# Kernel optimization log

Hardware: AMD Instinct MI355X
Metric: run time of the kernel (lower is better)

Reference implementation:

```python
import jax, jax.numpy as jnp
import numpy as np

HEADS = 8
EPS = 1e-5


def _attn_axis(x, axis, wq, wkv, wout, bout):
    # x: (B, C, X, Y, Z); self-attention along `axis`, channels at dim 1.
    perm = [0] + [d for d in (2, 3, 4) if d != axis] + [axis, 1]
    xp = jnp.transpose(x, perm)                    # (B, o1, o2, T, C)
    B, o1, o2, T, C = xp.shape
    xf = xp.reshape(B * o1 * o2, T, C)
    q = xf @ wq.T                                  # (Bf, T, C), no bias
    k, v = jnp.split(xf @ wkv.T, 2, axis=-1)
    e = C // HEADS
    sh = lambda t: t.reshape(t.shape[0], T, HEADS, e)
    q, k, v = sh(q), sh(k), sh(v)
    dots = jnp.einsum('bihe,bjhe->bhij', q, k) * (e ** -0.5)
    attn = jax.nn.softmax(dots, axis=-1)
    o = jnp.einsum('bhij,bjhe->bihe', attn, v).reshape(B * o1 * o2, T, C)
    o = (o @ wout.T + bout).reshape(B, o1, o2, T, C)
    inv = tuple(int(i) for i in np.argsort(perm))
    return jnp.transpose(o, inv)


def _ln(x, g, b):
    m = jnp.mean(x, -1, keepdims=True)
    v = jnp.mean((x - m) ** 2, -1, keepdims=True)
    return (x - m) * jax.lax.rsqrt(v + EPS) * g + b


def setup_inputs() -> dict:
    key = jax.random.key(0)
    B, C, X, Y, Z = 2, 128, 48, 48, 48
    ks = iter(jax.random.split(key, 32))
    n = lambda shape, s=0.02: jax.random.normal(next(ks), shape, jnp.float32) * s
    inp = {}
    inp['x'] = jax.random.normal(next(ks), (B, C, X, Y, Z), jnp.float32)
    inp['px'] = jax.random.normal(next(ks), (1, C, X, 1, 1), jnp.float32)
    inp['py'] = jax.random.normal(next(ks), (1, C, 1, Y, 1), jnp.float32)
    inp['pz'] = jax.random.normal(next(ks), (1, C, 1, 1, Z), jnp.float32)
    for i in range(3):
        inp[f'wq{i}'] = n((C, C))
        inp[f'wkv{i}'] = n((2 * C, C))
        inp[f'wout{i}'] = n((C, C))
        inp[f'bout{i}'] = jnp.zeros((C,), jnp.float32)
    inp['ln_g'] = jnp.ones((C,), jnp.float32)
    inp['ln_b'] = jnp.zeros((C,), jnp.float32)
    inp['w1'] = n((C, C)); inp['b1'] = jnp.zeros((C,), jnp.float32)
    inp['w2'] = n((C, C)); inp['b2'] = jnp.zeros((C,), jnp.float32)
    return inp


def reference(x, px, py, pz,
              wq0, wkv0, wout0, bout0,
              wq1, wkv1, wout1, bout1,
              wq2, wkv2, wout2, bout2,
              ln_g, ln_b, w1, b1, w2, b2):
    # source: x += pos_embedding(x); pos_embedding(x) returns x + px + py + pz
    x = x + (x + px + py + pz)
    a = (_attn_axis(x, 2, wq0, wkv0, wout0, bout0)
         + _attn_axis(x, 3, wq1, wkv1, wout1, bout1)
         + _attn_axis(x, 4, wq2, wkv2, wout2, bout2))
    x = a + x                                      # residual (dropout = identity)
    x = jnp.transpose(x, (0, 2, 3, 4, 1))          # channels last
    x = _ln(x, ln_g, ln_b)
    res = x
    h = jax.nn.relu(x @ w1.T + b1)
    h = h @ w2.T + b2
    x = _ln(h + res, ln_g, ln_b)                   # same LayerNorm weights reused
    return jnp.transpose(x, (0, 4, 1, 2, 3))
```

## Files before the change

kernel.cpp:

```cpp
#include <hip/hip_runtime.h>
#include <hip/hip_bf16.h>

typedef __attribute__((ext_vector_type(8))) short short8;
typedef __attribute__((ext_vector_type(4))) short short4v;
typedef __attribute__((ext_vector_type(4))) float floatx4;

#define XSTR 136
#define VSTR 56
#define SSTR 132
#define MSTR 129

static __device__ __forceinline__ short f2b(float f) {
    __hip_bfloat16 h = __float2bfloat16(f);
    return *reinterpret_cast<short*>(&h);
}
static __device__ __forceinline__ float b2f(short s) {
    unsigned int u = ((unsigned int)(unsigned short)s) << 16;
    return __uint_as_float(u);
}

__global__ __launch_bounds__(256) void prep_weights(
    const float* __restrict__ wq0, const float* __restrict__ wkv0,
    const float* __restrict__ wq1, const float* __restrict__ wkv1,
    const float* __restrict__ wq2, const float* __restrict__ wkv2,
    const float* __restrict__ wout0, const float* __restrict__ wout1,
    const float* __restrict__ wout2, const float* __restrict__ w1,
    const float* __restrict__ w2, short* __restrict__ dst)
{
    const int g = blockIdx.x * 256 + threadIdx.x;
    const float* wqs[3]  = { wq0, wq1, wq2 };
    const float* wkvs[3] = { wkv0, wkv1, wkv2 };
    const float* rest[5] = { wout0, wout1, wout2, w1, w2 };
    float val;
    if (g < 147456) {
        const int a = g / 49152, l = g % 49152;
        val = (l < 16384) ? wqs[a][l] : wkvs[a][l - 16384];
    } else {
        const int l = g - 147456;
        val = rest[l >> 14][l & 16383];
    }
    dst[g] = f2b(val);
}

__global__ __launch_bounds__(256) void prep_x2(
    const float* __restrict__ x, const float* __restrict__ px,
    const float* __restrict__ py, const float* __restrict__ pz,
    short* __restrict__ x2b)
{
    __shared__ float tile[128 * 49];
    const int s = blockIdx.x, tid = threadIdx.x;
    const int b = s / 2304, rr = s % 2304, xx = rr / 48, yy = rr % 48;
    for (int f = tid; f < 1536; f += 256) {
        const int c = f / 12, z4 = (f % 12) * 4;
        const floatx4 xv = *(const floatx4*)(x + (long)(b * 128 + c) * 110592 + xx * 2304 + yy * 48 + z4);
        const float pxy = px[c * 48 + xx] + py[c * 48 + yy];
        #pragma unroll
        for (int j = 0; j < 4; ++j)
            tile[c * 49 + z4 + j] = 2.0f * xv[j] + pxy + pz[c * 48 + z4 + j];
    }
    __syncthreads();
    const long tb = (long)b * 110592 + xx * 2304 + yy * 48;
    for (int f = tid; f < 1536; f += 256) {
        const int t = f >> 5, c4 = (f & 31) << 2;
        short4v pk;
        #pragma unroll
        for (int j = 0; j < 4; ++j) pk[j] = f2b(tile[(c4 + j) * 49 + t]);
        *(short4v*)(x2b + (tb + t) * 128 + c4) = pk;
    }
}

template<int AXIS, int ACC>
__global__ __launch_bounds__(512, 4)
void attn_axis(const short* __restrict__ x2b, const short* __restrict__ wcat,
               const short* __restrict__ woutb, const float* __restrict__ bout,
               short* __restrict__ Ab)
{
    __shared__ __align__(16) char SM[67840];
    short* xs  = (short*)SM;
    short* qs  = (short*)(SM + 13056);
    short* ks  = (short*)(SM + 26112);
    short* vs  = (short*)(SM + 39168);
    short* pb  = (short*)(SM + 53504);
    float* stg = (float*)(SM + 13056);

    const int tid  = threadIdx.x;
    const int lane = tid & 63;
    const int wave = tid >> 6;
    const int l15  = lane & 15;
    const int quad = lane >> 4;

    const int s = blockIdx.x;
    const int b = s / 2304, rr = s % 2304, u = rr / 48, v = rr % 48;
    long base; int stride;
    if (AXIS == 0) { base = (long)b * 110592 + u * 48   + v; stride = 2304; }
    else           { base = (long)b * 110592 + u * 2304 + v; stride = 48;   }

    short4v apre[3];
    if (ACC) {
        #pragma unroll
        for (int i = 0; i < 3; ++i) {
            const int f = tid + i * 512;
            const int t = f >> 5, c4 = (f & 31) << 2;
            apre[i] = *(const short4v*)(Ab + (base + (long)t * stride) * 128 + c4);
        }
    }
    short8 bcur[4], bnext[4];
    {
        const short* wp = wcat + (wave * 48 + l15) * 128 + quad * 8;
        #pragma unroll
        for (int k = 0; k < 4; ++k) bcur[k] = *(const short8*)(wp + k * 32);
    }

    for (int f = tid; f < 1536; f += 512) {
        const int t = f >> 5, c4 = (f & 31) << 2;
        *(short4v*)(xs + t * XSTR + c4) =
            *(const short4v*)(x2b + (base + (long)t * stride) * 128 + c4);
    }
    __syncthreads();

    short8 af[3][4];
    #pragma unroll
    for (int mt = 0; mt < 3; ++mt)
        #pragma unroll
        for (int k = 0; k < 4; ++k)
            af[mt][k] = *(const short8*)(xs + (mt * 16 + l15) * XSTR + k * 32 + quad * 8);

    for (int nti = 0; nti < 3; ++nti) {
        const int nt = wave * 3 + nti;
        const int n  = nt * 16 + l15;
        if (nti < 2) {
            const short* wp = wcat + ((nt + 1) * 16 + l15) * 128 + quad * 8;
            #pragma unroll
            for (int k = 0; k < 4; ++k) bnext[k] = *(const short8*)(wp + k * 32);
        }
        floatx4 acc[3] = {{0,0,0,0},{0,0,0,0},{0,0,0,0}};
        #pragma unroll
        for (int mt = 0; mt < 3; ++mt)
            #pragma unroll
            for (int k = 0; k < 4; ++k)
                acc[mt] = __builtin_amdgcn_mfma_f32_16x16x32_bf16(af[mt][k], bcur[k], acc[mt], 0, 0, 0);
        #pragma unroll
        for (int mt = 0; mt < 3; ++mt) {
            const int rbase = mt * 16 + quad * 4;
            if (n < 128) {
                #pragma unroll
                for (int g = 0; g < 4; ++g)
                    qs[(rbase + g) * XSTR + n] = f2b(acc[mt][g] * 0.25f);
            } else if (n < 256) {
                #pragma unroll
                for (int g = 0; g < 4; ++g)
                    ks[(rbase + g) * XSTR + (n - 128)] = f2b(acc[mt][g]);
            } else {
                short4v pk;
                #pragma unroll
                for (int g = 0; g < 4; ++g) pk[g] = f2b(acc[mt][g]);
                *(short4v*)(vs + (n - 256) * VSTR + rbase) = pk;
            }
        }
        #pragma unroll
        for (int k = 0; k < 4; ++k) bcur[k] = bnext[k];
    }
    __syncthreads();

    short* pbw = pb + wave * (16 * VSTR);
    const short8 Z8 = {0,0,0,0,0,0,0,0};
    for (int task = wave; task < 24; task += 8) {
        const int h  = task / 3;
        const int mt = task - h * 3;
        const int hb = h * 16;
        short8 aq = Z8;
        if (quad < 2) aq = *(const short8*)(qs + (mt * 16 + l15) * XSTR + hb + quad * 8);
        floatx4 sc[3];
        #pragma unroll
        for (int nt = 0; nt < 3; ++nt) {
            short8 bk = Z8;
            if (quad < 2) bk = *(const short8*)(ks + (nt * 16 + l15) * XSTR + hb + quad * 8);
            floatx4 z = {0,0,0,0};
            sc[nt] = __builtin_amdgcn_mfma_f32_16x16x32_bf16(aq, bk, z, 0, 0, 0);
        }
        #pragma unroll
        for (int g = 0; g < 4; ++g) {
            float m = fmaxf(fmaxf(sc[0][g], sc[1][g]), sc[2][g]);
            m = fmaxf(m, __shfl_xor(m, 1, 64));
            m = fmaxf(m, __shfl_xor(m, 2, 64));
            m = fmaxf(m, __shfl_xor(m, 4, 64));
            m = fmaxf(m, __shfl_xor(m, 8, 64));
            const float e0 = __expf(sc[0][g] - m);
            const float e1 = __expf(sc[1][g] - m);
            const float e2 = __expf(sc[2][g] - m);
            float ssum = e0 + e1 + e2;
            ssum += __shfl_xor(ssum, 1, 64);
            ssum += __shfl_xor(ssum, 2, 64);
            ssum += __shfl_xor(ssum, 4, 64);
            ssum += __shfl_xor(ssum, 8, 64);
            const float inv = 1.0f / ssum;
            short* prow = pbw + (quad * 4 + g) * VSTR;
            prow[l15]      = f2b(e0 * inv);
            prow[16 + l15] = f2b(e1 * inv);
            prow[32 + l15] = f2b(e2 * inv);
        }
        floatx4 o = {0,0,0,0};
        {
            short8 ap = *(const short8*)(pbw + l15 * VSTR + quad * 8);
            short8 bv = *(const short8*)(vs + (hb + l15) * VSTR + quad * 8);
            o = __builtin_amdgcn_mfma_f32_16x16x32_bf16(ap, bv, o, 0, 0, 0);
            short8 ap1 = Z8, bv1 = Z8;
            if (quad < 2) {
                ap1 = *(const short8*)(pbw + l15 * VSTR + 32 + quad * 8);
                bv1 = *(const short8*)(vs + (hb + l15) * VSTR + 32 + quad * 8);
            }
            o = __builtin_amdgcn_mfma_f32_16x16x32_bf16(ap1, bv1, o, 0, 0, 0);
        }
        #pragma unroll
        for (int g = 0; g < 4; ++g)
            xs[(mt * 16 + quad * 4 + g) * XSTR + hb + l15] = f2b(o[g]);
    }
    __syncthreads();

    #pragma unroll
    for (int mt = 0; mt < 3; ++mt)
        #pragma unroll
        for (int k = 0; k < 4; ++k)
            af[mt][k] = *(const short8*)(xs + (mt * 16 + l15) * XSTR + k * 32 + quad * 8);

    {
        const int n = wave * 16 + l15;
        short8 bf_[4];
        #pragma unroll
        for (int k = 0; k < 4; ++k)
            bf_[k] = *(const short8*)(woutb + n * 128 + k * 32 + quad * 8);
        floatx4 acc[3] = {{0,0,0,0},{0,0,0,0},{0,0,0,0}};
        #pragma unroll
        for (int mt = 0; mt < 3; ++mt)
            #pragma unroll
            for (int k = 0; k < 4; ++k)
                acc[mt] = __builtin_amdgcn_mfma_f32_16x16x32_bf16(af[mt][k], bf_[k], acc[mt], 0, 0, 0);
        const float bo = bout[n];
        #pragma unroll
        for (int mt = 0; mt < 3; ++mt)
            #pragma unroll
            for (int g = 0; g < 4; ++g)
                stg[(mt * 16 + quad * 4 + g) * SSTR + n] = acc[mt][g] + bo;
    }
    __syncthreads();

    #pragma unroll
    for (int i = 0; i < 3; ++i) {
        const int f = tid + i * 512;
        const int t = f >> 5, c4 = (f & 31) << 2;
        const long gi = (base + (long)t * stride) * 128 + c4;
        const floatx4 vv = *(const floatx4*)(stg + t * SSTR + c4);
        short4v out4;
        if (ACC) {
            #pragma unroll
            for (int j = 0; j < 4; ++j) out4[j] = f2b(b2f(apre[i][j]) + vv[j]);
        } else {
            #pragma unroll
            for (int j = 0; j < 4; ++j) out4[j] = f2b(vv[j]);
        }
        *(short4v*)(Ab + gi) = out4;
    }
}

static __device__ __forceinline__ void ln_stats129(const float* xr, float* mean_,
                                                   float* rstd_, int tid)
{
    if (tid < 192) {
        const int r = tid >> 2, p = tid & 3;
        const float* row = xr + r * MSTR + p * 32;
        float s1 = 0.f, s2 = 0.f;
        #pragma unroll
        for (int c = 0; c < 32; ++c) { const float xv = row[c]; s1 += xv; s2 += xv * xv; }
        s1 += __shfl_xor(s1, 1, 64); s1 += __shfl_xor(s1, 2, 64);
        s2 += __shfl_xor(s2, 1, 64); s2 += __shfl_xor(s2, 2, 64);
        if (p == 0) {
            const float m = s1 * (1.f / 128.f);
            mean_[r] = m;
            rstd_[r] = rsqrtf(s2 * (1.f / 128.f) - m * m + 1e-5f);
        }
    }
}

__global__ __launch_bounds__(512, 4)
void attn2_mlp(const short* __restrict__ x2b, const short* __restrict__ Ab,
               const short* __restrict__ wcat, const short* __restrict__ woutb,
               const float* __restrict__ bout,
               const float* __restrict__ ln_g, const float* __restrict__ ln_b,
               const short* __restrict__ w1b, const float* __restrict__ b1,
               const short* __restrict__ w2b, const float* __restrict__ b2,
               float* __restrict__ out)
{
    __shared__ __align__(16) char SM[70272];
    short* xs   = (short*)SM;
    short* qs   = (short*)(SM + 13056);
    short* ks   = (short*)(SM + 26112);
    short* vs   = (short*)(SM + 39168);
    short* pb   = (short*)(SM + 53504);
    short* ob   = xs;
    float* xr   = (float*)(SM + 13056);
    short* lnb  = (short*)(SM + 39168);
    short* hbuf = xs;
    float* gs   = (float*)(SM + 67840);
    float* bs   = (float*)(SM + 68352);
    float* b1s  = (float*)(SM + 68864);
    float* b2s  = (float*)(SM + 69376);
    float* mean_ = (float*)(SM + 69888);
    float* rstd_ = (float*)(SM + 70080);

    const int tid  = threadIdx.x;
    const int lane = tid & 63;
    const int wave = tid >> 6;
    const int l15  = lane & 15;
    const int quad = lane >> 4;

    const int s = blockIdx.x;
    const int b = s / 2304, rr = s % 2304, xx = rr / 48, yy = rr % 48;
    const long tb = (long)b * 110592 + xx * 2304 + yy * 48;

    short4v apre[3];
    #pragma unroll
    for (int i = 0; i < 3; ++i) {
        const int f = tid + i * 512;
        const int t = f >> 5, c4 = (f & 31) << 2;
        apre[i] = *(const short4v*)(Ab + (tb + t) * 128 + c4);
    }
    short8 bcur[4], bnext[4];
    {
        const short* wp = wcat + (wave * 48 + l15) * 128 + quad * 8;
        #pragma unroll
        for (int k = 0; k < 4; ++k) bcur[k] = *(const short8*)(wp + k * 32);
    }

    if (tid < 128) {
        gs[tid] = ln_g[tid]; bs[tid] = ln_b[tid];
        b1s[tid] = b1[tid];  b2s[tid] = b2[tid];
    }
    short4v xpre[3];
    #pragma unroll
    for (int i = 0; i < 3; ++i) {
        const int f = tid + i * 512;
        const int t = f >> 5, c4 = (f & 31) << 2;
        xpre[i] = *(const short4v*)(x2b + (tb + t) * 128 + c4);
        *(short4v*)(xs + t * XSTR + c4) = xpre[i];
    }
    __syncthreads();

    short8 af[3][4];
    #pragma unroll
    for (int mt = 0; mt < 3; ++mt)
        #pragma unroll
        for (int k = 0; k < 4; ++k)
            af[mt][k] = *(const short8*)(xs + (mt * 16 + l15) * XSTR + k * 32 + quad * 8);

    for (int nti = 0; nti < 3; ++nti) {
        const int nt = wave * 3 + nti;
        const int n  = nt * 16 + l15;
        if (nti < 2) {
            const short* wp = wcat + ((nt + 1) * 16 + l15) * 128 + quad * 8;
            #pragma unroll
            for (int k = 0; k < 4; ++k) bnext[k] = *(const short8*)(wp + k * 32);
        }
        floatx4 acc[3] = {{0,0,0,0},{0,0,0,0},{0,0,0,0}};
        #pragma unroll
        for (int mt = 0; mt < 3; ++mt)
            #pragma unroll
            for (int k = 0; k < 4; ++k)
                acc[mt] = __builtin_amdgcn_mfma_f32_16x16x32_bf16(af[mt][k], bcur[k], acc[mt], 0, 0, 0);
        #pragma unroll
        for (int mt = 0; mt < 3; ++mt) {
            const int rbase = mt * 16 + quad * 4;
            if (n < 128) {
                #pragma unroll
                for (int g = 0; g < 4; ++g)
                    qs[(rbase + g) * XSTR + n] = f2b(acc[mt][g] * 0.25f);
            } else if (n < 256) {
                #pragma unroll
                for (int g = 0; g < 4; ++g)
                    ks[(rbase + g) * XSTR + (n - 128)] = f2b(acc[mt][g]);
            } else {
                short4v pk;
                #pragma unroll
                for (int g = 0; g < 4; ++g) pk[g] = f2b(acc[mt][g]);
                *(short4v*)(vs + (n - 256) * VSTR + rbase) = pk;
            }
        }
        #pragma unroll
        for (int k = 0; k < 4; ++k) bcur[k] = bnext[k];
    }
    __syncthreads();

    short* pbw = pb + wave * (16 * VSTR);
    const short8 Z8 = {0,0,0,0,0,0,0,0};
    for (int task = wave; task < 24; task += 8) {
        const int h  = task / 3;
        const int mt = task - h * 3;
        const int hb = h * 16;
        short8 aq = Z8;
        if (quad < 2) aq = *(const short8*)(qs + (mt * 16 + l15) * XSTR + hb + quad * 8);
        floatx4 sc[3];
        #pragma unroll
        for (int nt = 0; nt < 3; ++nt) {
            short8 bk = Z8;
            if (quad < 2) bk = *(const short8*)(ks + (nt * 16 + l15) * XSTR + hb + quad * 8);
            floatx4 z = {0,0,0,0};
            sc[nt] = __builtin_amdgcn_mfma_f32_16x16x32_bf16(aq, bk, z, 0, 0, 0);
        }
        #pragma unroll
        for (int g = 0; g < 4; ++g) {
            float m = fmaxf(fmaxf(sc[0][g], sc[1][g]), sc[2][g]);
            m = fmaxf(m, __shfl_xor(m, 1, 64));
            m = fmaxf(m, __shfl_xor(m, 2, 64));
            m = fmaxf(m, __shfl_xor(m, 4, 64));
            m = fmaxf(m, __shfl_xor(m, 8, 64));
            const float e0 = __expf(sc[0][g] - m);
            const float e1 = __expf(sc[1][g] - m);
            const float e2 = __expf(sc[2][g] - m);
            float ssum = e0 + e1 + e2;
            ssum += __shfl_xor(ssum, 1, 64);
            ssum += __shfl_xor(ssum, 2, 64);
            ssum += __shfl_xor(ssum, 4, 64);
            ssum += __shfl_xor(ssum, 8, 64);
            const float inv = 1.0f / ssum;
            short* prow = pbw + (quad * 4 + g) * VSTR;
            prow[l15]      = f2b(e0 * inv);
            prow[16 + l15] = f2b(e1 * inv);
            prow[32 + l15] = f2b(e2 * inv);
        }
        floatx4 o = {0,0,0,0};
        {
            short8 ap = *(const short8*)(pbw + l15 * VSTR + quad * 8);
            short8 bv = *(const short8*)(vs + (hb + l15) * VSTR + quad * 8);
            o = __builtin_amdgcn_mfma_f32_16x16x32_bf16(ap, bv, o, 0, 0, 0);
            short8 ap1 = Z8, bv1 = Z8;
            if (quad < 2) {
                ap1 = *(const short8*)(pbw + l15 * VSTR + 32 + quad * 8);
                bv1 = *(const short8*)(vs + (hb + l15) * VSTR + 32 + quad * 8);
            }
            o = __builtin_amdgcn_mfma_f32_16x16x32_bf16(ap1, bv1, o, 0, 0, 0);
        }
        #pragma unroll
        for (int g = 0; g < 4; ++g)
            ob[(mt * 16 + quad * 4 + g) * XSTR + hb + l15] = f2b(o[g]);
    }
    __syncthreads();

    #pragma unroll
    for (int mt = 0; mt < 3; ++mt)
        #pragma unroll
        for (int k = 0; k < 4; ++k)
            af[mt][k] = *(const short8*)(ob + (mt * 16 + l15) * XSTR + k * 32 + quad * 8);
    {
        const int n = wave * 16 + l15;
        short8 bf_[4];
        #pragma unroll
        for (int k = 0; k < 4; ++k)
            bf_[k] = *(const short8*)(woutb + n * 128 + k * 32 + quad * 8);
        floatx4 acc[3] = {{0,0,0,0},{0,0,0,0},{0,0,0,0}};
        #pragma unroll
        for (int mt = 0; mt < 3; ++mt)
            #pragma unroll
            for (int k = 0; k < 4; ++k)
                acc[mt] = __builtin_amdgcn_mfma_f32_16x16x32_bf16(af[mt][k], bf_[k], acc[mt], 0, 0, 0);
        const float bo = bout[n];
        #pragma unroll
        for (int mt = 0; mt < 3; ++mt)
            #pragma unroll
            for (int g = 0; g < 4; ++g)
                xr[(mt * 16 + quad * 4 + g) * MSTR + n] = acc[mt][g] + bo;
    }
    __syncthreads();

    #pragma unroll
    for (int i = 0; i < 3; ++i) {
        const int f = tid + i * 512;
        const int t = f >> 5, c4 = (f & 31) << 2;
        #pragma unroll
        for (int j = 0; j < 4; ++j)
            xr[t * MSTR + c4 + j] += b2f(apre[i][j]) + b2f(xpre[i][j]);
    }
    __syncthreads();

    ln_stats129(xr, mean_, rstd_, tid);
    __syncthreads();
    for (int f = tid; f < 6144; f += 512) {
        const int t = f >> 7, c = f & 127;
        lnb[t * XSTR + c] = f2b((xr[t * MSTR + c] - mean_[t]) * rstd_[t] * gs[c] + bs[c]);
    }
    __syncthreads();

    #pragma unroll
    for (int mt = 0; mt < 3; ++mt)
        #pragma unroll
        for (int k = 0; k < 4; ++k)
            af[mt][k] = *(const short8*)(lnb + (mt * 16 + l15) * XSTR + k * 32 + quad * 8);
    {
        const int n = wave * 16 + l15;
        short8 bf_[4];
        #pragma unroll
        for (int k = 0; k < 4; ++k)
            bf_[k] = *(const short8*)(w1b + n * 128 + k * 32 + quad * 8);
        floatx4 acc[3] = {{0,0,0,0},{0,0,0,0},{0,0,0,0}};
        #pragma unroll
        for (int mt = 0; mt < 3; ++mt)
            #pragma unroll
            for (int k = 0; k < 4; ++k)
                acc[mt] = __builtin_amdgcn_mfma_f32_16x16x32_bf16(af[mt][k], bf_[k], acc[mt], 0, 0, 0);
        const float bb = b1s[n];
        #pragma unroll
        for (int mt = 0; mt < 3; ++mt)
            #pragma unroll
            for (int g = 0; g < 4; ++g)
                hbuf[(mt * 16 + quad * 4 + g) * XSTR + n] = f2b(fmaxf(acc[mt][g] + bb, 0.f));
    }
    __syncthreads();

    #pragma unroll
    for (int mt = 0; mt < 3; ++mt)
        #pragma unroll
        for (int k = 0; k < 4; ++k)
            af[mt][k] = *(const short8*)(hbuf + (mt * 16 + l15) * XSTR + k * 32 + quad * 8);
    {
        const int n = wave * 16 + l15;
        short8 bf_[4];
        #pragma unroll
        for (int k = 0; k < 4; ++k)
            bf_[k] = *(const short8*)(w2b + n * 128 + k * 32 + quad * 8);
        floatx4 acc[3] = {{0,0,0,0},{0,0,0,0},{0,0,0,0}};
        #pragma unroll
        for (int mt = 0; mt < 3; ++mt)
            #pragma unroll
            for (int k = 0; k < 4; ++k)
                acc[mt] = __builtin_amdgcn_mfma_f32_16x16x32_bf16(af[mt][k], bf_[k], acc[mt], 0, 0, 0);
        const float bb = b2s[n];
        #pragma unroll
        for (int mt = 0; mt < 3; ++mt)
            #pragma unroll
            for (int g = 0; g < 4; ++g) {
                const int t = mt * 16 + quad * 4 + g;
                const float ln1 = (xr[t * MSTR + n] - mean_[t]) * rstd_[t] * gs[n] + bs[n];
                xr[t * MSTR + n] = acc[mt][g] + bb + ln1;
            }
    }
    __syncthreads();
    ln_stats129(xr, mean_, rstd_, tid);
    __syncthreads();

    for (int f = tid; f < 1536; f += 512) {
        const int c = f / 12, z4 = (f % 12) * 4;
        floatx4 o4;
        #pragma unroll
        for (int j = 0; j < 4; ++j)
            o4[j] = (xr[(z4 + j) * MSTR + c] - mean_[z4 + j]) * rstd_[z4 + j] * gs[c] + bs[c];
        *(floatx4*)(out + (long)(b * 128 + c) * 110592 + xx * 2304 + yy * 48 + z4) = o4;
    }
}

extern "C" void kernel_launch(void* const* d_in, const int* in_sizes, int n_in,
                              void* d_out, int out_size, void* d_ws, size_t ws_size,
                              hipStream_t stream)
{
    const float* x    = (const float*)d_in[0];
    const float* px   = (const float*)d_in[1];
    const float* py   = (const float*)d_in[2];
    const float* pz   = (const float*)d_in[3];
    const float* wq[3]   = { (const float*)d_in[4],  (const float*)d_in[8],  (const float*)d_in[12] };
    const float* wkv[3]  = { (const float*)d_in[5],  (const float*)d_in[9],  (const float*)d_in[13] };
    const float* wout[3] = { (const float*)d_in[6],  (const float*)d_in[10], (const float*)d_in[14] };
    const float* bout[3] = { (const float*)d_in[7],  (const float*)d_in[11], (const float*)d_in[15] };
    const float* ln_g = (const float*)d_in[16];
    const float* ln_b = (const float*)d_in[17];
    const float* w1   = (const float*)d_in[18];
    const float* b1   = (const float*)d_in[19];
    const float* w2   = (const float*)d_in[20];
    const float* b2   = (const float*)d_in[21];

    short* Ab  = (short*)d_ws;
    short* wb  = (short*)((char*)d_ws + 56623104);
    short* x2b = (short*)((char*)d_ws + 57081856);

    prep_weights<<<896, 256, 0, stream>>>(wq[0], wkv[0], wq[1], wkv[1], wq[2], wkv[2],
                                          wout[0], wout[1], wout[2], w1, w2, wb);
    prep_x2<<<4608, 256, 0, stream>>>(x, px, py, pz, x2b);

    attn_axis<0, 0><<<4608, 512, 0, stream>>>(x2b, wb,         wb + 147456, bout[0], Ab);
    attn_axis<1, 1><<<4608, 512, 0, stream>>>(x2b, wb + 49152, wb + 163840, bout[1], Ab);

    attn2_mlp<<<4608, 512, 0, stream>>>(x2b, Ab, wb + 98304, wb + 180224, bout[2],
                                        ln_g, ln_b, wb + 196608, b1, wb + 212992, b2,
                                        (float*)d_out);
}
```

Measured before the change: 645.5 us.

## Assign each wave one head's QKV columns to drop the projection-to-attention barrier

```diff
diff --git a/kernel.cpp b/kernel.cpp
--- a/kernel.cpp
+++ b/kernel.cpp
@@ -6,7 +6,7 @@
 typedef __attribute__((ext_vector_type(4))) float floatx4;
 
 #define XSTR 136
-#define VSTR 56
+#define VSTR 48
 #define SSTR 132
 #define MSTR 129
 
@@ -75,12 +75,13 @@
                const short* __restrict__ woutb, const float* __restrict__ bout,
                short* __restrict__ Ab)
 {
-    __shared__ __align__(16) char SM[67840];
+    __shared__ __align__(16) char SM[76800];
     short* xs  = (short*)SM;
     short* qs  = (short*)(SM + 13056);
     short* ks  = (short*)(SM + 26112);
     short* vs  = (short*)(SM + 39168);
-    short* pb  = (short*)(SM + 53504);
+    short* pb  = (short*)(SM + 51456);
+    short* ob  = (short*)(SM + 63744);
     float* stg = (float*)(SM + 13056);
 
     const int tid  = threadIdx.x;
@@ -106,7 +107,7 @@
     }
     short8 bcur[4], bnext[4];
     {
-        const short* wp = wcat + (wave * 48 + l15) * 128 + quad * 8;
+        const short* wp = wcat + (wave * 16 + l15) * 128 + quad * 8;
         #pragma unroll
         for (int k = 0; k < 4; ++k) bcur[k] = *(const short8*)(wp + k * 32);
     }
@@ -125,14 +126,11 @@
         for (int k = 0; k < 4; ++k)
             af[mt][k] = *(const short8*)(xs + (mt * 16 + l15) * XSTR + k * 32 + quad * 8);
 
-    for (int nti = 0; nti < 3; ++nti) {
-        const int nt = wave * 3 + nti;
-        const int n  = nt * 16 + l15;
-        if (nti < 2) {
-            const short* wp = wcat + ((nt + 1) * 16 + l15) * 128 + quad * 8;
-            #pragma unroll
-            for (int k = 0; k < 4; ++k) bnext[k] = *(const short8*)(wp + k * 32);
-        }
+    const int n0 = wave * 16 + l15;
+    {
+        const short* wp = wcat + ((wave + 8) * 16 + l15) * 128 + quad * 8;
+        #pragma unroll
+        for (int k = 0; k < 4; ++k) bnext[k] = *(const short8*)(wp + k * 32);
         floatx4 acc[3] = {{0,0,0,0},{0,0,0,0},{0,0,0,0}};
         #pragma unroll
         for (int mt = 0; mt < 3; ++mt)
@@ -142,52 +140,73 @@
         #pragma unroll
         for (int mt = 0; mt < 3; ++mt) {
             const int rbase = mt * 16 + quad * 4;
-            if (n < 128) {
-                #pragma unroll
-                for (int g = 0; g < 4; ++g)
-                    qs[(rbase + g) * XSTR + n] = f2b(acc[mt][g] * 0.25f);
-            } else if (n < 256) {
-                #pragma unroll
-                for (int g = 0; g < 4; ++g)
-                    ks[(rbase + g) * XSTR + (n - 128)] = f2b(acc[mt][g]);
-            } else {
-                short4v pk;
-                #pragma unroll
-                for (int g = 0; g < 4; ++g) pk[g] = f2b(acc[mt][g]);
-                *(short4v*)(vs + (n - 256) * VSTR + rbase) = pk;
-            }
-        }
-        #pragma unroll
-        for (int k = 0; k < 4; ++k) bcur[k] = bnext[k];
-    }
-    __syncthreads();
+            #pragma unroll
+            for (int g = 0; g < 4; ++g)
+                qs[(rbase + g) * XSTR + n0] = f2b(acc[mt][g] * 0.25f);
+        }
+    }
+    {
+        const short* wp = wcat + ((wave + 16) * 16 + l15) * 128 + quad * 8;
+        #pragma unroll
+        for (int k = 0; k < 4; ++k) bcur[k] = *(const short8*)(wp + k * 32);
+        floatx4 acc[3] = {{0,0,0,0},{0,0,0,0},{0,0,0,0}};
+        #pragma unroll
+        for (int mt = 0; mt < 3; ++mt)
+            #pragma unroll
+            for (int k = 0; k < 4; ++k)
+                acc[mt] = __builtin_amdgcn_mfma_f32_16x16x32_bf16(af[mt][k], bnext[k], acc[mt], 0, 0, 0);
+        #pragma unroll
+        for (int mt = 0; mt < 3; ++mt) {
+            const int rbase = mt * 16 + quad * 4;
+            #pragma unroll
+            for (int g = 0; g < 4; ++g)
+                ks[(rbase + g) * XSTR + n0] = f2b(acc[mt][g]);
+        }
+    }
+    {
+        floatx4 acc[3] = {{0,0,0,0},{0,0,0,0},{0,0,0,0}};
+        #pragma unroll
+        for (int mt = 0; mt < 3; ++mt)
+            #pragma unroll
+            for (int k = 0; k < 4; ++k)
+                acc[mt] = __builtin_amdgcn_mfma_f32_16x16x32_bf16(af[mt][k], bcur[k], acc[mt], 0, 0, 0);
+        #pragma unroll
+        for (int mt = 0; mt < 3; ++mt) {
+            short4v pk;
+            #pragma unroll
+            for (int g = 0; g < 4; ++g) pk[g] = f2b(acc[mt][g]);
+            *(short4v*)(vs + n0 * VSTR + mt * 16 + quad * 4) = pk;
+        }
+    }
 
     short* pbw = pb + wave * (16 * VSTR);
     const short8 Z8 = {0,0,0,0,0,0,0,0};
-    for (int task = wave; task < 24; task += 8) {
-        const int h  = task / 3;
-        const int mt = task - h * 3;
-        const int hb = h * 16;
+    const int hb = wave * 16;
+    short8 bk[3], bv0, bv1;
+    #pragma unroll
+    for (int nt = 0; nt < 3; ++nt) {
+        bk[nt] = Z8;
+        if (quad < 2) bk[nt] = *(const short8*)(ks + (nt * 16 + l15) * XSTR + hb + quad * 8);
+    }
+    bv0 = *(const short8*)(vs + (hb + l15) * VSTR + quad * 8);
+    bv1 = Z8;
+    if (quad < 2) bv1 = *(const short8*)(vs + (hb + l15) * VSTR + 32 + quad * 8);
+
+    #pragma unroll
+    for (int mt = 0; mt < 3; ++mt) {
         short8 aq = Z8;
         if (quad < 2) aq = *(const short8*)(qs + (mt * 16 + l15) * XSTR + hb + quad * 8);
         floatx4 sc[3];
         #pragma unroll
         for (int nt = 0; nt < 3; ++nt) {
-            short8 bk = Z8;
-            if (quad < 2) bk = *(const short8*)(ks + (nt * 16 + l15) * XSTR + hb + quad * 8);
             floatx4 z = {0,0,0,0};
-            sc[nt] = __builtin_amdgcn_mfma_f32_16x16x32_bf16(aq, bk, z, 0, 0, 0);
+            sc[nt] = __builtin_amdgcn_mfma_f32_16x16x32_bf16(aq, bk[nt], z, 0, 0, 0);
         }
         #pragma unroll
         for (int g = 0; g < 4; ++g) {
-            float m = fmaxf(fmaxf(sc[0][g], sc[1][g]), sc[2][g]);
-            m = fmaxf(m, __shfl_xor(m, 1, 64));
-            m = fmaxf(m, __shfl_xor(m, 2, 64));
-            m = fmaxf(m, __shfl_xor(m, 4, 64));
-            m = fmaxf(m, __shfl_xor(m, 8, 64));
-            const float e0 = __expf(sc[0][g] - m);
-            const float e1 = __expf(sc[1][g] - m);
-            const float e2 = __expf(sc[2][g] - m);
+            const float e0 = __expf(sc[0][g]);
+            const float e1 = __expf(sc[1][g]);
+            const float e2 = __expf(sc[2][g]);
             float ssum = e0 + e1 + e2;
             ssum += __shfl_xor(ssum, 1, 64);
             ssum += __shfl_xor(ssum, 2, 64);
@@ -202,18 +221,14 @@
         floatx4 o = {0,0,0,0};
         {
             short8 ap = *(const short8*)(pbw + l15 * VSTR + quad * 8);
-            short8 bv = *(const short8*)(vs + (hb + l15) * VSTR + quad * 8);
-            o = __builtin_amdgcn_mfma_f32_16x16x32_bf16(ap, bv, o, 0, 0, 0);
-            short8 ap1 = Z8, bv1 = Z8;
-            if (quad < 2) {
-                ap1 = *(const short8*)(pbw + l15 * VSTR + 32 + quad * 8);
-                bv1 = *(const short8*)(vs + (hb + l15) * VSTR + 32 + quad * 8);
-            }
+            o = __builtin_amdgcn_mfma_f32_16x16x32_bf16(ap, bv0, o, 0, 0, 0);
+            short8 ap1 = Z8;
+            if (quad < 2) ap1 = *(const short8*)(pbw + l15 * VSTR + 32 + quad * 8);
             o = __builtin_amdgcn_mfma_f32_16x16x32_bf16(ap1, bv1, o, 0, 0, 0);
         }
         #pragma unroll
         for (int g = 0; g < 4; ++g)
-            xs[(mt * 16 + quad * 4 + g) * XSTR + hb + l15] = f2b(o[g]);
+            ob[(mt * 16 + quad * 4 + g) * XSTR + hb + l15] = f2b(o[g]);
     }
     __syncthreads();
 
@@ -221,8 +236,7 @@
     for (int mt = 0; mt < 3; ++mt)
         #pragma unroll
         for (int k = 0; k < 4; ++k)
-            af[mt][k] = *(const short8*)(xs + (mt * 16 + l15) * XSTR + k * 32 + quad * 8);
-
+            af[mt][k] = *(const short8*)(ob + (mt * 16 + l15) * XSTR + k * 32 + quad * 8);
     {
         const int n = wave * 16 + l15;
         short8 bf_[4];
@@ -270,7 +284,10 @@
         const float* row = xr + r * MSTR + p * 32;
         float s1 = 0.f, s2 = 0.f;
         #pragma unroll
-        for (int c = 0; c < 32; ++c) { const float xv = row[c]; s1 += xv; s2 += xv * xv; }
+        for (int c0 = 0; c0 < 32; ++c0) {
+            const float xv = row[(c0 + p * 8) & 31];
+            s1 += xv; s2 += xv * xv;
+        }
         s1 += __shfl_xor(s1, 1, 64); s1 += __shfl_xor(s1, 2, 64);
         s2 += __shfl_xor(s2, 1, 64); s2 += __shfl_xor(s2, 2, 64);
         if (p == 0) {
@@ -290,22 +307,22 @@
                const short* __restrict__ w2b, const float* __restrict__ b2,
                float* __restrict__ out)
 {
-    __shared__ __align__(16) char SM[70272];
+    __shared__ __align__(16) char SM[79232];
     short* xs   = (short*)SM;
     short* qs   = (short*)(SM + 13056);
     short* ks   = (short*)(SM + 26112);
     short* vs   = (short*)(SM + 39168);
-    short* pb   = (short*)(SM + 53504);
-    short* ob   = xs;
+    short* pb   = (short*)(SM + 51456);
+    short* ob   = (short*)(SM + 63744);
     float* xr   = (float*)(SM + 13056);
     short* lnb  = (short*)(SM + 39168);
-    short* hbuf = xs;
-    float* gs   = (float*)(SM + 67840);
-    float* bs   = (float*)(SM + 68352);
-    float* b1s  = (float*)(SM + 68864);
-    float* b2s  = (float*)(SM + 69376);
-    float* mean_ = (float*)(SM + 69888);
-    float* rstd_ = (float*)(SM + 70080);
+    short* hbuf = (short*)(SM + 63744);
+    float* gs   = (float*)(SM + 76800);
+    float* bs   = (float*)(SM + 77312);
+    float* b1s  = (float*)(SM + 77824);
+    float* b2s  = (float*)(SM + 78336);
+    float* mean_ = (float*)(SM + 78848);
+    float* rstd_ = (float*)(SM + 79040);
 
     const int tid  = threadIdx.x;
     const int lane = tid & 63;
@@ -326,7 +343,7 @@
     }
     short8 bcur[4], bnext[4];
     {
-        const short* wp = wcat + (wave * 48 + l15) * 128 + quad * 8;
+        const short* wp = wcat + (wave * 16 + l15) * 128 + quad * 8;
         #pragma unroll
         for (int k = 0; k < 4; ++k) bcur[k] = *(const short8*)(wp + k * 32);
     }
@@ -352,14 +369,11 @@
         for (int k = 0; k < 4; ++k)
             af[mt][k] = *(const short8*)(xs + (mt * 16 + l15) * XSTR + k * 32 + quad * 8);
 
-    for (int nti = 0; nti < 3; ++nti) {
-        const int nt = wave * 3 + nti;
-        const int n  = nt * 16 + l15;
-        if (nti < 2) {
-            const short* wp = wcat + ((nt + 1) * 16 + l15) * 128 + quad * 8;
-            #pragma unroll
-            for (int k = 0; k < 4; ++k) bnext[k] = *(const short8*)(wp + k * 32);
-        }
+    const int n0 = wave * 16 + l15;
+    {
+        const short* wp = wcat + ((wave + 8) * 16 + l15) * 128 + quad * 8;
+        #pragma unroll
+        for (int k = 0; k < 4; ++k) bnext[k] = *(const short8*)(wp + k * 32);
         floatx4 acc[3] = {{0,0,0,0},{0,0,0,0},{0,0,0,0}};
         #pragma unroll
         for (int mt = 0; mt < 3; ++mt)
@@ -369,52 +383,73 @@
         #pragma unroll
         for (int mt = 0; mt < 3; ++mt) {
             const int rbase = mt * 16 + quad * 4;
-            if (n < 128) {
-                #pragma unroll
-                for (int g = 0; g < 4; ++g)
-                    qs[(rbase + g) * XSTR + n] = f2b(acc[mt][g] * 0.25f);
-            } else if (n < 256) {
-                #pragma unroll
-                for (int g = 0; g < 4; ++g)
-                    ks[(rbase + g) * XSTR + (n - 128)] = f2b(acc[mt][g]);
-            } else {
-                short4v pk;
-                #pragma unroll
-                for (int g = 0; g < 4; ++g) pk[g] = f2b(acc[mt][g]);
-                *(short4v*)(vs + (n - 256) * VSTR + rbase) = pk;
-            }
-        }
-        #pragma unroll
-        for (int k = 0; k < 4; ++k) bcur[k] = bnext[k];
-    }
-    __syncthreads();
+            #pragma unroll
+            for (int g = 0; g < 4; ++g)
+                qs[(rbase + g) * XSTR + n0] = f2b(acc[mt][g] * 0.25f);
+        }
+    }
+    {
+        const short* wp = wcat + ((wave + 16) * 16 + l15) * 128 + quad * 8;
+        #pragma unroll
+        for (int k = 0; k < 4; ++k) bcur[k] = *(const short8*)(wp + k * 32);
+        floatx4 acc[3] = {{0,0,0,0},{0,0,0,0},{0,0,0,0}};
+        #pragma unroll
+        for (int mt = 0; mt < 3; ++mt)
+            #pragma unroll
+            for (int k = 0; k < 4; ++k)
+                acc[mt] = __builtin_amdgcn_mfma_f32_16x16x32_bf16(af[mt][k], bnext[k], acc[mt], 0, 0, 0);
+        #pragma unroll
+        for (int mt = 0; mt < 3; ++mt) {
+            const int rbase = mt * 16 + quad * 4;
+            #pragma unroll
+            for (int g = 0; g < 4; ++g)
+                ks[(rbase + g) * XSTR + n0] = f2b(acc[mt][g]);
+        }
+    }
+    {
+        floatx4 acc[3] = {{0,0,0,0},{0,0,0,0},{0,0,0,0}};
+        #pragma unroll
+        for (int mt = 0; mt < 3; ++mt)
+            #pragma unroll
+            for (int k = 0; k < 4; ++k)
+                acc[mt] = __builtin_amdgcn_mfma_f32_16x16x32_bf16(af[mt][k], bcur[k], acc[mt], 0, 0, 0);
+        #pragma unroll
+        for (int mt = 0; mt < 3; ++mt) {
+            short4v pk;
+            #pragma unroll
+            for (int g = 0; g < 4; ++g) pk[g] = f2b(acc[mt][g]);
+            *(short4v*)(vs + n0 * VSTR + mt * 16 + quad * 4) = pk;
+        }
+    }
 
     short* pbw = pb + wave * (16 * VSTR);
     const short8 Z8 = {0,0,0,0,0,0,0,0};
-    for (int task = wave; task < 24; task += 8) {
-        const int h  = task / 3;
-        const int mt = task - h * 3;
-        const int hb = h * 16;
+    const int hb = wave * 16;
+    short8 bk[3], bv0, bv1;
+    #pragma unroll
+    for (int nt = 0; nt < 3; ++nt) {
+        bk[nt] = Z8;
+        if (quad < 2) bk[nt] = *(const short8*)(ks + (nt * 16 + l15) * XSTR + hb + quad * 8);
+    }
+    bv0 = *(const short8*)(vs + (hb + l15) * VSTR + quad * 8);
+    bv1 = Z8;
+    if (quad < 2) bv1 = *(const short8*)(vs + (hb + l15) * VSTR + 32 + quad * 8);
+
+    #pragma unroll
+    for (int mt = 0; mt < 3; ++mt) {
         short8 aq = Z8;
         if (quad < 2) aq = *(const short8*)(qs + (mt * 16 + l15) * XSTR + hb + quad * 8);
         floatx4 sc[3];
         #pragma unroll
         for (int nt = 0; nt < 3; ++nt) {
-            short8 bk = Z8;
-            if (quad < 2) bk = *(const short8*)(ks + (nt * 16 + l15) * XSTR + hb + quad * 8);
             floatx4 z = {0,0,0,0};
-            sc[nt] = __builtin_amdgcn_mfma_f32_16x16x32_bf16(aq, bk, z, 0, 0, 0);
+            sc[nt] = __builtin_amdgcn_mfma_f32_16x16x32_bf16(aq, bk[nt], z, 0, 0, 0);
         }
         #pragma unroll
         for (int g = 0; g < 4; ++g) {
-            float m = fmaxf(fmaxf(sc[0][g], sc[1][g]), sc[2][g]);
-            m = fmaxf(m, __shfl_xor(m, 1, 64));
-            m = fmaxf(m, __shfl_xor(m, 2, 64));
-            m = fmaxf(m, __shfl_xor(m, 4, 64));
-            m = fmaxf(m, __shfl_xor(m, 8, 64));
-            const float e0 = __expf(sc[0][g] - m);
-            const float e1 = __expf(sc[1][g] - m);
-            const float e2 = __expf(sc[2][g] - m);
+            const float e0 = __expf(sc[0][g]);
+            const float e1 = __expf(sc[1][g]);
+            const float e2 = __expf(sc[2][g]);
             float ssum = e0 + e1 + e2;
             ssum += __shfl_xor(ssum, 1, 64);
             ssum += __shfl_xor(ssum, 2, 64);
@@ -429,13 +464,9 @@
         floatx4 o = {0,0,0,0};
         {
             short8 ap = *(const short8*)(pbw + l15 * VSTR + quad * 8);
-            short8 bv = *(const short8*)(vs + (hb + l15) * VSTR + quad * 8);
-            o = __builtin_amdgcn_mfma_f32_16x16x32_bf16(ap, bv, o, 0, 0, 0);
-            short8 ap1 = Z8, bv1 = Z8;
-            if (quad < 2) {
-                ap1 = *(const short8*)(pbw + l15 * VSTR + 32 + quad * 8);
-                bv1 = *(const short8*)(vs + (hb + l15) * VSTR + 32 + quad * 8);
-            }
+            o = __builtin_amdgcn_mfma_f32_16x16x32_bf16(ap, bv0, o, 0, 0, 0);
+            short8 ap1 = Z8;
+            if (quad < 2) ap1 = *(const short8*)(pbw + l15 * VSTR + 32 + quad * 8);
             o = __builtin_amdgcn_mfma_f32_16x16x32_bf16(ap1, bv1, o, 0, 0, 0);
         }
         #pragma unroll
@@ -474,14 +505,26 @@
     for (int i = 0; i < 3; ++i) {
         const int f = tid + i * 512;
         const int t = f >> 5, c4 = (f & 31) << 2;
-        #pragma unroll
-        for (int j = 0; j < 4; ++j)
-            xr[t * MSTR + c4 + j] += b2f(apre[i][j]) + b2f(xpre[i][j]);
-    }
-    __syncthreads();
-
-    ln_stats129(xr, mean_, rstd_, tid);
-    __syncthreads();
+        float s1 = 0.f, s2 = 0.f;
+        #pragma unroll
+        for (int j = 0; j < 4; ++j) {
+            const float vv = xr[t * MSTR + c4 + j] + b2f(apre[i][j]) + b2f(xpre[i][j]);
+            xr[t * MSTR + c4 + j] = vv;
+            s1 += vv; s2 += vv * vv;
+        }
+        s1 += __shfl_xor(s1, 1, 64);  s2 += __shfl_xor(s2, 1, 64);
+        s1 += __shfl_xor(s1, 2, 64);  s2 += __shfl_xor(s2, 2, 64);
+        s1 += __shfl_xor(s1, 4, 64);  s2 += __shfl_xor(s2, 4, 64);
+        s1 += __shfl_xor(s1, 8, 64);  s2 += __shfl_xor(s2, 8, 64);
+        s1 += __shfl_xor(s1, 16, 64); s2 += __shfl_xor(s2, 16, 64);
+        if ((lane & 31) == 0) {
+            const float m = s1 * (1.f / 128.f);
+            mean_[t] = m;
+            rstd_[t] = rsqrtf(s2 * (1.f / 128.f) - m * m + 1e-5f);
+        }
+    }
+    __syncthreads();
+
     for (int f = tid; f < 6144; f += 512) {
         const int t = f >> 7, c = f & 127;
         lnb[t * XSTR + c] = f2b((xr[t * MSTR + c] - mean_[t]) * rstd_[t] * gs[c] + bs[c]);
```

After: 601.6 us. 6.8% less time.
